# Kernel optimization log

Hardware: AMD Instinct MI355X
Metric: run time of the kernel (lower is better)

The kernel has to match this reference:

```python
import jax, jax.numpy as jnp
import numpy as np

N_NODES = 100000
N_EDGES = 1600000
N_FEAT = 100
HIDDEN = 64
N_CLASSES = 47


def setup_inputs() -> dict:
    key = jax.random.key(0)
    k1, k2, k3, k4 = jax.random.split(key, 4)
    x = jax.random.normal(k1, (N_NODES, N_FEAT), dtype=jnp.float32)
    edge_index = jax.random.randint(k2, (2, N_EDGES), 0, N_NODES, dtype=jnp.int64)
    # Glorot-style init for GCNConv weights; zero bias (PyG default)
    W0 = jax.random.normal(k3, (N_FEAT, HIDDEN), dtype=jnp.float32) * (1.0 / np.sqrt(N_FEAT))
    b0 = jnp.zeros((HIDDEN,), dtype=jnp.float32)
    W1 = jax.random.normal(k4, (HIDDEN, N_CLASSES), dtype=jnp.float32) * (1.0 / np.sqrt(HIDDEN))
    b1 = jnp.zeros((N_CLASSES,), dtype=jnp.float32)
    return {"x": x, "edge_index": edge_index, "W0": W0, "b0": b0, "W1": W1, "b1": b1}


def _gcn_norm(edge_index, n_nodes):
    # PyG gcn_norm with add_self_loops=True, edge_weight=1
    loop = jnp.arange(n_nodes, dtype=edge_index.dtype)
    row = jnp.concatenate([edge_index[0], loop])  # source nodes
    col = jnp.concatenate([edge_index[1], loop])  # destination nodes
    ones = jnp.ones(row.shape[0], dtype=jnp.float32)
    deg = jax.ops.segment_sum(ones, col, num_segments=n_nodes)
    dinv = jnp.where(deg > 0, jax.lax.rsqrt(deg), 0.0)
    norm = dinv[row] * dinv[col]  # [E + N]
    return row, col, norm


def _gcn_conv(x, W, b, row, col, norm, n_nodes):
    # GCNConv: transform, then gather-scale-scatter aggregate, then bias
    xw = x @ W                                   # [N, out]
    msg = norm[:, None] * xw[row]                # [E+N, out]
    out = jax.ops.segment_sum(msg, col, num_segments=n_nodes)
    return out + b


def reference(x, edge_index, W0, b0, W1, b1):
    n_nodes = x.shape[0]
    row, col, norm = _gcn_norm(edge_index, n_nodes)  # same graph -> same norm per layer (cached)
    h = _gcn_conv(x, W0, b0, row, col, norm, n_nodes)
    h = jax.nn.relu(h)  # dropout is identity in eval mode
    out = _gcn_conv(h, W1, b1, row, col, norm, n_nodes)
    return out
```

## Files before the change

### kernel.cpp

```cpp
#include <hip/hip_runtime.h>
#include <hip/hip_fp16.h>

#define N_NODES   100000
#define N_EDGES   1600000
#define N_FEAT    100
#define HIDDEN    64
#define N_CLASSES 47
#define ZPAD      48
#define NBIN      ((N_NODES + 255) / 256)
#define SBLK      512
#define CHUNK     (N_EDGES / SBLK)
#define NHIST     (NBIN * SBLK)
#define WT0_ELEMS (HIDDEN * 128)
#define WT1_ELEMS (ZPAD * 64)
#define WPREP_N   (WT0_ELEMS + WT1_ELEMS)

typedef _Float16 f16x8 __attribute__((ext_vector_type(8)));
typedef float f32x4 __attribute__((ext_vector_type(4)));


__global__ __launch_bounds__(512) void k_gscan1(const int* __restrict__ in,
                                                int* __restrict__ out,
                                                int* __restrict__ sums, int n) {
    __shared__ int tmp[512];
    int i = blockIdx.x * 512 + threadIdx.x;
    int v = (i < n) ? in[i] : 0;
    tmp[threadIdx.x] = v;
    __syncthreads();
    for (int off = 1; off < 512; off <<= 1) {
        int t = (threadIdx.x >= off) ? tmp[threadIdx.x - off] : 0;
        __syncthreads();
        tmp[threadIdx.x] += t;
        __syncthreads();
    }
    if (i < n) out[i] = tmp[threadIdx.x] - v;
    if (threadIdx.x == 511) sums[blockIdx.x] = tmp[511];
}

__global__ __launch_bounds__(512) void k_gscan2(int* __restrict__ sums, int nb) {
    __shared__ int tmp[512];
    int i = threadIdx.x;
    int v = (i < nb) ? sums[i] : 0;
    tmp[i] = v;
    __syncthreads();
    for (int off = 1; off < 512; off <<= 1) {
        int t = (i >= off) ? tmp[i - off] : 0;
        __syncthreads();
        tmp[i] += t;
        __syncthreads();
    }
    if (i < nb) sums[i] = tmp[i] - v;
}


__global__ __launch_bounds__(256) void k_hist(const int* __restrict__ ecol,
                                              int* __restrict__ gh,
                                              const float* __restrict__ W0,
                                              const float* __restrict__ W1,
                                              __half* __restrict__ wt0,
                                              __half* __restrict__ wt1) {
    int wi = blockIdx.x * 256 + threadIdx.x;
    if (wi < WT0_ELEMS) {
        int n = wi >> 7, k = wi & 127;
        wt0[wi] = __float2half((k < N_FEAT) ? W0[k * HIDDEN + n] : 0.0f);
    } else if (wi < WPREP_N) {
        int j = wi - WT0_ELEMS;
        int n = j >> 6, k = j & 63;
        wt1[j] = __float2half((n < N_CLASSES) ? W1[k * N_CLASSES + n] : 0.0f);
    }

    __shared__ int lh[NBIN];
    int b = blockIdx.x, t = threadIdx.x;
    for (int i = t; i < NBIN; i += 256) lh[i] = 0;
    __syncthreads();
    int e0 = b * CHUNK;
    for (int i = t; i < CHUNK; i += 256)
        atomicAdd(&lh[ecol[e0 + i] >> 8], 1);
    __syncthreads();
    for (int i = t; i < NBIN; i += 256) gh[i * SBLK + b] = lh[i];
}

__global__ __launch_bounds__(256) void k_radix_scatter(
    const int* __restrict__ erow, const int* __restrict__ ecol,
    const int* __restrict__ gpos, const int* __restrict__ hsums,
    int* __restrict__ pairs) {
    __shared__ int lc[NBIN];
    int b = blockIdx.x, t = threadIdx.x;
    for (int i = t; i < NBIN; i += 256) lc[i] = gpos[i * SBLK + b] + hsums[i];
    __syncthreads();
    int e0 = b * CHUNK;
    for (int i = t; i < CHUNK; i += 256) {
        int e = e0 + i;
        int r = erow[e], c = ecol[e];
        int pos = atomicAdd(&lc[c >> 8], 1);
        pairs[pos] = r | ((c & 255) << 17);
    }
}

__global__ __launch_bounds__(1024) void k_binfinish(
    const int* __restrict__ gpos, const int* __restrict__ hsums,
    const int* __restrict__ pairs,
    int* __restrict__ rp, float* __restrict__ dinv, int* __restrict__ eidx) {
    __shared__ int cnt[256];
    __shared__ int tmp[256];
    int b = blockIdx.x, t = threadIdx.x;
    int n0 = b << 8;
    int beg = gpos[b * SBLK] + hsums[b];
    int end = (b + 1 < NBIN) ? gpos[(b + 1) * SBLK] + hsums[b + 1] : N_EDGES;

    if (t < 256) cnt[t] = 0;
    __syncthreads();
    for (int i = beg + t; i < end; i += 1024)
        atomicAdd(&cnt[(pairs[i] >> 17) & 255], 1);
    __syncthreads();
    int v = 0;
    if (t < 256) { v = cnt[t]; tmp[t] = v; }
    __syncthreads();
    for (int off = 1; off < 256; off <<= 1) {
        int u = (t < 256 && t >= off) ? tmp[t - off] : 0;
        __syncthreads();
        if (t < 256) tmp[t] += u;
        __syncthreads();
    }
    if (t < 256) {
        int rpv = beg + tmp[t] - v;
        int n = n0 + t;
        if (n < N_NODES) {
            rp[n] = rpv;
            dinv[n] = rsqrtf(1.0f + (float)v);
        }
        cnt[t] = rpv;
    }
    if (b == NBIN - 1 && t == 0) rp[N_NODES] = N_EDGES;
    __syncthreads();
    for (int i = beg + t; i < end; i += 1024) {
        int p = pairs[i];
        int pos = atomicAdd(&cnt[(p >> 17) & 255], 1);
        eidx[pos] = p & 0x1FFFF;
    }
}

__global__ __launch_bounds__(256) void k_gemm1(
    const float* __restrict__ x, const __half* __restrict__ wt0,
    const float* __restrict__ dinv, __half* __restrict__ yh) {
    int w = threadIdx.x >> 6, l = threadIdx.x & 63;
    int g = l >> 4, c16 = l & 15;
    int row = blockIdx.x * 64 + w * 16 + c16;
    int rl = (row < N_NODES) ? row : (N_NODES - 1);
    const float* xr = x + (size_t)rl * N_FEAT;

    f16x8 a[4];
    #pragma unroll
    for (int s = 0; s < 4; ++s) {
        int k0 = 32 * s + 8 * g;
        float4 f0 = (k0 + 3 < N_FEAT) ? *(const float4*)(xr + k0)
                                      : make_float4(0.f, 0.f, 0.f, 0.f);
        float4 f1 = (k0 + 7 < N_FEAT) ? *(const float4*)(xr + k0 + 4)
                                      : make_float4(0.f, 0.f, 0.f, 0.f);
        a[s][0] = (_Float16)f0.x; a[s][1] = (_Float16)f0.y;
        a[s][2] = (_Float16)f0.z; a[s][3] = (_Float16)f0.w;
        a[s][4] = (_Float16)f1.x; a[s][5] = (_Float16)f1.y;
        a[s][6] = (_Float16)f1.z; a[s][7] = (_Float16)f1.w;
    }
    f32x4 acc0 = {0,0,0,0}, acc1 = {0,0,0,0}, acc2 = {0,0,0,0}, acc3 = {0,0,0,0};
    #pragma unroll
    for (int s = 0; s < 4; ++s) {
        int ko = 32 * s + 8 * g;
        f16x8 b0 = *(const f16x8*)(wt0 + (0 * 16 + c16) * 128 + ko);
        f16x8 b1 = *(const f16x8*)(wt0 + (1 * 16 + c16) * 128 + ko);
        f16x8 b2 = *(const f16x8*)(wt0 + (2 * 16 + c16) * 128 + ko);
        f16x8 b3 = *(const f16x8*)(wt0 + (3 * 16 + c16) * 128 + ko);
        acc0 = __builtin_amdgcn_mfma_f32_16x16x32_f16(a[s], b0, acc0, 0, 0, 0);
        acc1 = __builtin_amdgcn_mfma_f32_16x16x32_f16(a[s], b1, acc1, 0, 0, 0);
        acc2 = __builtin_amdgcn_mfma_f32_16x16x32_f16(a[s], b2, acc2, 0, 0, 0);
        acc3 = __builtin_amdgcn_mfma_f32_16x16x32_f16(a[s], b3, acc3, 0, 0, 0);
    }
    int orow = blockIdx.x * 64 + w * 16 + 4 * g;
    #pragma unroll
    for (int r = 0; r < 4; ++r) {
        int rr = orow + r;
        float di = (rr < N_NODES) ? dinv[rr] : 0.0f;
        size_t base = (size_t)rr * HIDDEN + c16;
        yh[base +  0] = __float2half(di * acc0[r]);
        yh[base + 16] = __float2half(di * acc1[r]);
        yh[base + 32] = __float2half(di * acc2[r]);
        yh[base + 48] = __float2half(di * acc3[r]);
    }
}

__global__ __launch_bounds__(256) void k_agg0(
    const int* __restrict__ rp, const int* __restrict__ eidx,
    const float* __restrict__ dinv, const __half* __restrict__ yh,
    const float* __restrict__ b0, const __half* __restrict__ wt1,
    __half* __restrict__ zh) {
    __shared__ __half hs[16][64];
    int t = blockIdx.x * 256 + threadIdx.x;
    int n = t >> 5;
    int hl = threadIdx.x & 31;
    int nl = threadIdx.x >> 5;

    ((__half2*)hs)[256 + threadIdx.x] = __floats2half2_rn(0.f, 0.f);

    int beg = rp[n], end = rp[n + 1];
    int deg = end - beg;
    int se = (beg + hl < end) ? eidx[beg + hl] : 0;
    const __half2* yh2 = (const __half2*)yh;
    float2 fs = __half22float2(yh2[(size_t)n * 32 + hl]);
    float ax = fs.x, ay = fs.y;
    int m = deg < 32 ? deg : 32;
    int base = threadIdx.x & 32;
    const __half2 hz = __floats2half2_rn(0.f, 0.f);

    {
        __half2 h[16];
        #pragma unroll
        for (int k = 0; k < 16; ++k) {
            int s = __shfl(se, base + k);
            h[k] = yh2[(size_t)s * 32 + hl];
        }
        #pragma unroll
        for (int k = 0; k < 16; ++k) h[k] = (m > k) ? h[k] : hz;
        #pragma unroll
        for (int s2 = 8; s2 >= 1; s2 >>= 1) {
            #pragma unroll
            for (int k = 0; k < s2; ++k) h[k] = __hadd2(h[2 * k], h[2 * k + 1]);
        }
        float2 bs = __half22float2(h[0]);
        ax += bs.x; ay += bs.y;
    }
    if (m > 16) {
        __half2 h[16];
        #pragma unroll
        for (int k = 0; k < 16; ++k) {
            int s = __shfl(se, base + 16 + k);
            h[k] = yh2[(size_t)s * 32 + hl];
        }
        #pragma unroll
        for (int k = 0; k < 16; ++k) h[k] = (m > 16 + k) ? h[k] : hz;
        #pragma unroll
        for (int s2 = 8; s2 >= 1; s2 >>= 1) {
            #pragma unroll
            for (int k = 0; k < s2; ++k) h[k] = __hadd2(h[2 * k], h[2 * k + 1]);
        }
        float2 bs = __half22float2(h[0]);
        ax += bs.x; ay += bs.y;
    }
    if (deg > 32) {
        for (int e = beg + 32; e < end; ++e) {
            int s = eidx[e];
            float2 fv = __half22float2(yh2[(size_t)s * 32 + hl]);
            ax += fv.x; ay += fv.y;
        }
    }
    float di = dinv[n];
    float2 b2 = ((const float2*)b0)[hl];
    float o0 = fmaxf(di * ax + b2.x, 0.0f);
    float o1 = fmaxf(di * ay + b2.y, 0.0f);
    ((__half2*)hs)[nl * 32 + hl] = __floats2half2_rn(o0, o1);
    __syncthreads();

    if (threadIdx.x < 64) {
        int l = threadIdx.x;
        int g = l >> 4, c16 = l & 15;
        f16x8 a0 = *(const f16x8*)(&hs[c16][8 * g]);
        f16x8 a1 = *(const f16x8*)(&hs[c16][32 + 8 * g]);
        f32x4 acc0 = {0,0,0,0}, acc1 = {0,0,0,0}, acc2 = {0,0,0,0};
        #pragma unroll
        for (int s = 0; s < 2; ++s) {
            int ko = 32 * s + 8 * g;
            f16x8 b0f = *(const f16x8*)(wt1 + (0 * 16 + c16) * 64 + ko);
            f16x8 b1f = *(const f16x8*)(wt1 + (1 * 16 + c16) * 64 + ko);
            f16x8 b2f = *(const f16x8*)(wt1 + (2 * 16 + c16) * 64 + ko);
            f16x8 av = s ? a1 : a0;
            acc0 = __builtin_amdgcn_mfma_f32_16x16x32_f16(av, b0f, acc0, 0, 0, 0);
            acc1 = __builtin_amdgcn_mfma_f32_16x16x32_f16(av, b1f, acc1, 0, 0, 0);
            acc2 = __builtin_amdgcn_mfma_f32_16x16x32_f16(av, b2f, acc2, 0, 0, 0);
        }
        if (g < 2) {
            int nrow = blockIdx.x * 8 + 4 * g;
            #pragma unroll
            for (int r = 0; r < 4; ++r) {
                float dr = dinv[nrow + r];
                size_t bz = (size_t)(nrow + r) * ZPAD + c16;
                zh[bz +  0] = __float2half(dr * acc0[r]);
                zh[bz + 16] = __float2half(dr * acc1[r]);
                zh[bz + 32] = __float2half(dr * acc2[r]);
            }
        }
    }
}

__global__ __launch_bounds__(256) void k_agg1(
    const int* __restrict__ rp, const int* __restrict__ eidx,
    const float* __restrict__ dinv, const __half* __restrict__ zh,
    const float* __restrict__ b1, float* __restrict__ out) {
    int t = blockIdx.x * 256 + threadIdx.x;
    int n = t >> 5;
    int hl = threadIdx.x & 31;
    if (n >= N_NODES) return;
    int beg = rp[n], end = rp[n + 1];
    int deg = end - beg;
    int se = (beg + hl < end) ? eidx[beg + hl] : 0;
    const __half2* zh2 = (const __half2*)zh;
    float ax = 0.0f, ay = 0.0f;
    if (hl < 24) {
        float2 f = __half22float2(zh2[(size_t)n * 24 + hl]);
        ax = f.x; ay = f.y;
    }
    int m = deg < 32 ? deg : 32;
    int base = threadIdx.x & 32;
    const __half2 hz = __floats2half2_rn(0.f, 0.f);

    {
        int sidx[16];
        #pragma unroll
        for (int k = 0; k < 16; ++k) sidx[k] = __shfl(se, base + k);
        if (hl < 24) {
            __half2 h[16];
            #pragma unroll
            for (int k = 0; k < 16; ++k) h[k] = zh2[(size_t)sidx[k] * 24 + hl];
            #pragma unroll
            for (int k = 0; k < 16; ++k) h[k] = (m > k) ? h[k] : hz;
            #pragma unroll
            for (int s2 = 8; s2 >= 1; s2 >>= 1) {
                #pragma unroll
                for (int k = 0; k < s2; ++k) h[k] = __hadd2(h[2 * k], h[2 * k + 1]);
            }
            float2 bs = __half22float2(h[0]);
            ax += bs.x; ay += bs.y;
        }
    }
    if (m > 16) {
        int sidx[16];
        #pragma unroll
        for (int k = 0; k < 16; ++k) sidx[k] = __shfl(se, base + 16 + k);
        if (hl < 24) {
            __half2 h[16];
            #pragma unroll
            for (int k = 0; k < 16; ++k) h[k] = zh2[(size_t)sidx[k] * 24 + hl];
            #pragma unroll
            for (int k = 0; k < 16; ++k) h[k] = (m > 16 + k) ? h[k] : hz;
            #pragma unroll
            for (int s2 = 8; s2 >= 1; s2 >>= 1) {
                #pragma unroll
                for (int k = 0; k < s2; ++k) h[k] = __hadd2(h[2 * k], h[2 * k + 1]);
            }
            float2 bs = __half22float2(h[0]);
            ax += bs.x; ay += bs.y;
        }
    }
    if (deg > 32) {
        for (int e = beg + 32; e < end; ++e) {
            int s = eidx[e];
            if (hl < 24) {
                float2 fv = __half22float2(zh2[(size_t)s * 24 + hl]);
                ax += fv.x; ay += fv.y;
            }
        }
    }
    if (hl < 24) {
        float di = dinv[n];
        out[(size_t)n * N_CLASSES + 2 * hl] = di * ax + b1[2 * hl];
        if (hl < 23)
            out[(size_t)n * N_CLASSES + 2 * hl + 1] = di * ay + b1[2 * hl + 1];
    }
}

extern "C" void kernel_launch(void* const* d_in, const int* in_sizes, int n_in,
                              void* d_out, int out_size, void* d_ws, size_t ws_size,
                              hipStream_t stream) {
    const float* x  = (const float*)d_in[0];
    const int*   ei = (const int*)d_in[1];
    const float* W0 = (const float*)d_in[2];
    const float* b0 = (const float*)d_in[3];
    const float* W1 = (const float*)d_in[4];
    const float* b1 = (const float*)d_in[5];
    float* out = (float*)d_out;

    char* ws = (char*)d_ws;
    float*  dinv  = (float*)(ws);
    int*    rp    = (int*)(ws + 412 * 1024);
    int*    hsums = (int*)(ws + 824 * 1024);
    int*    gh    = (int*)(ws + 828 * 1024);
    int*    gpos  = (int*)(ws + 1612 * 1024);
    __half* wt0   = (__half*)(ws + 2400 * 1024);
    __half* wt1   = (__half*)(ws + 2420 * 1024);
    int*    eidx  = (int*)(ws + 2428 * 1024);
    __half* yh    = (__half*)(ws + 10ull * 1024 * 1024);
    __half* zh    = (__half*)(ws + 23ull * 1024 * 1024);
    int*    pairs = (int*)zh;

    const int* erow = ei;
    const int* ecol = ei + N_EDGES;

    k_hist  <<<SBLK, 256, 0, stream>>>(ecol, gh, W0, W1, wt0, wt1);
    k_gscan1<<<NBIN, 512, 0, stream>>>(gh, gpos, hsums, NHIST);
    k_gscan2<<<1, 512, 0, stream>>>(hsums, NBIN);
    k_radix_scatter<<<SBLK, 256, 0, stream>>>(erow, ecol, gpos, hsums, pairs);
    k_binfinish<<<NBIN, 1024, 0, stream>>>(gpos, hsums, pairs, rp, dinv, eidx);

    k_gemm1<<<(N_NODES + 63) / 64, 256, 0, stream>>>(x, wt0, dinv, yh);
    k_agg0 <<<(N_NODES * 32) / 256, 256, 0, stream>>>(rp, eidx, dinv, yh, b0, wt1, zh);

    k_agg1 <<<(N_NODES * 32) / 256, 256, 0, stream>>>(rp, eidx, dinv, zh, b1, out);
}
```

Baseline: 131.4 us.

## Fold block-sum scan into consumers, pad z rows to 64 halves, widen scatter blocks

New measurement: 127.5 us (median of 2 runs). 3.0% less time.

```diff
diff --git a/kernel.cpp b/kernel.cpp
--- a/kernel.cpp
+++ b/kernel.cpp
@@ -6,13 +6,13 @@
 #define N_FEAT    100
 #define HIDDEN    64
 #define N_CLASSES 47
-#define ZPAD      48
+#define ZROWH     64
 #define NBIN      ((N_NODES + 255) / 256)
 #define SBLK      512
 #define CHUNK     (N_EDGES / SBLK)
 #define NHIST     (NBIN * SBLK)
 #define WT0_ELEMS (HIDDEN * 128)
-#define WT1_ELEMS (ZPAD * 64)
+#define WT1_ELEMS (48 * 64)
 #define WPREP_N   (WT0_ELEMS + WT1_ELEMS)
 
 typedef _Float16 f16x8 __attribute__((ext_vector_type(8)));
@@ -35,21 +35,6 @@
     }
     if (i < n) out[i] = tmp[threadIdx.x] - v;
     if (threadIdx.x == 511) sums[blockIdx.x] = tmp[511];
-}
-
-__global__ __launch_bounds__(512) void k_gscan2(int* __restrict__ sums, int nb) {
-    __shared__ int tmp[512];
-    int i = threadIdx.x;
-    int v = (i < nb) ? sums[i] : 0;
-    tmp[i] = v;
-    __syncthreads();
-    for (int off = 1; off < 512; off <<= 1) {
-        int t = (i >= off) ? tmp[i - off] : 0;
-        __syncthreads();
-        tmp[i] += t;
-        __syncthreads();
-    }
-    if (i < nb) sums[i] = tmp[i] - v;
 }
 
 
@@ -80,16 +65,26 @@
     for (int i = t; i < NBIN; i += 256) gh[i * SBLK + b] = lh[i];
 }
 
-__global__ __launch_bounds__(256) void k_radix_scatter(
+__global__ __launch_bounds__(512) void k_radix_scatter(
     const int* __restrict__ erow, const int* __restrict__ ecol,
-    const int* __restrict__ gpos, const int* __restrict__ hsums,
+    const int* __restrict__ gpos, const int* __restrict__ bsums,
     int* __restrict__ pairs) {
     __shared__ int lc[NBIN];
+    __shared__ int sc[512];
     int b = blockIdx.x, t = threadIdx.x;
-    for (int i = t; i < NBIN; i += 256) lc[i] = gpos[i * SBLK + b] + hsums[i];
+    int bv = (t < NBIN) ? bsums[t] : 0;
+    sc[t] = bv;
+    __syncthreads();
+    for (int off = 1; off < 512; off <<= 1) {
+        int u = (t >= off) ? sc[t - off] : 0;
+        __syncthreads();
+        sc[t] += u;
+        __syncthreads();
+    }
+    if (t < NBIN) lc[t] = gpos[t * SBLK + b] + sc[t] - bv;
     __syncthreads();
     int e0 = b * CHUNK;
-    for (int i = t; i < CHUNK; i += 256) {
+    for (int i = t; i < CHUNK; i += 512) {
         int e = e0 + i;
         int r = erow[e], c = ecol[e];
         int pos = atomicAdd(&lc[c >> 8], 1);
@@ -98,15 +93,27 @@
 }
 
 __global__ __launch_bounds__(1024) void k_binfinish(
-    const int* __restrict__ gpos, const int* __restrict__ hsums,
+    const int* __restrict__ gpos, const int* __restrict__ bsums,
     const int* __restrict__ pairs,
     int* __restrict__ rp, float* __restrict__ dinv, int* __restrict__ eidx) {
     __shared__ int cnt[256];
     __shared__ int tmp[256];
+    __shared__ int sc[512];
     int b = blockIdx.x, t = threadIdx.x;
     int n0 = b << 8;
-    int beg = gpos[b * SBLK] + hsums[b];
-    int end = (b + 1 < NBIN) ? gpos[(b + 1) * SBLK] + hsums[b + 1] : N_EDGES;
+    int bv = 0;
+    if (t < 512) { bv = (t < NBIN) ? bsums[t] : 0; sc[t] = bv; }
+    __syncthreads();
+    for (int off = 1; off < 512; off <<= 1) {
+        int u = (t < 512 && t >= off) ? sc[t - off] : 0;
+        __syncthreads();
+        if (t < 512) sc[t] += u;
+        __syncthreads();
+    }
+    if (t < 512) sc[t] -= bv;
+    __syncthreads();
+    int beg = gpos[b * SBLK] + sc[b];
+    int end = (b + 1 < NBIN) ? gpos[(b + 1) * SBLK] + sc[b + 1] : N_EDGES;
 
     if (t < 256) cnt[t] = 0;
     __syncthreads();
@@ -281,7 +288,7 @@
             #pragma unroll
             for (int r = 0; r < 4; ++r) {
                 float dr = dinv[nrow + r];
-                size_t bz = (size_t)(nrow + r) * ZPAD + c16;
+                size_t bz = (size_t)(nrow + r) * ZROWH + c16;
                 zh[bz +  0] = __float2half(dr * acc0[r]);
                 zh[bz + 16] = __float2half(dr * acc1[r]);
                 zh[bz + 32] = __float2half(dr * acc2[r]);
@@ -304,7 +311,7 @@
     const __half2* zh2 = (const __half2*)zh;
     float ax = 0.0f, ay = 0.0f;
     if (hl < 24) {
-        float2 f = __half22float2(zh2[(size_t)n * 24 + hl]);
+        float2 f = __half22float2(zh2[(size_t)n * 32 + hl]);
         ax = f.x; ay = f.y;
     }
     int m = deg < 32 ? deg : 32;
@@ -318,7 +325,7 @@
         if (hl < 24) {
             __half2 h[16];
             #pragma unroll
-            for (int k = 0; k < 16; ++k) h[k] = zh2[(size_t)sidx[k] * 24 + hl];
+            for (int k = 0; k < 16; ++k) h[k] = zh2[(size_t)sidx[k] * 32 + hl];
             #pragma unroll
             for (int k = 0; k < 16; ++k) h[k] = (m > k) ? h[k] : hz;
             #pragma unroll
@@ -337,7 +344,7 @@
         if (hl < 24) {
             __half2 h[16];
             #pragma unroll
-            for (int k = 0; k < 16; ++k) h[k] = zh2[(size_t)sidx[k] * 24 + hl];
+            for (int k = 0; k < 16; ++k) h[k] = zh2[(size_t)sidx[k] * 32 + hl];
             #pragma unroll
             for (int k = 0; k < 16; ++k) h[k] = (m > 16 + k) ? h[k] : hz;
             #pragma unroll
@@ -353,7 +360,7 @@
         for (int e = beg + 32; e < end; ++e) {
             int s = eidx[e];
             if (hl < 24) {
-                float2 fv = __half22float2(zh2[(size_t)s * 24 + hl]);
+                float2 fv = __half22float2(zh2[(size_t)s * 32 + hl]);
                 ax += fv.x; ay += fv.y;
             }
         }
@@ -380,7 +387,7 @@
     char* ws = (char*)d_ws;
     float*  dinv  = (float*)(ws);
     int*    rp    = (int*)(ws + 412 * 1024);
-    int*    hsums = (int*)(ws + 824 * 1024);
+    int*    bsums = (int*)(ws + 824 * 1024);
     int*    gh    = (int*)(ws + 828 * 1024);
     int*    gpos  = (int*)(ws + 1612 * 1024);
     __half* wt0   = (__half*)(ws + 2400 * 1024);
@@ -394,10 +401,9 @@
     const int* ecol = ei + N_EDGES;
 
     k_hist  <<<SBLK, 256, 0, stream>>>(ecol, gh, W0, W1, wt0, wt1);
-    k_gscan1<<<NBIN, 512, 0, stream>>>(gh, gpos, hsums, NHIST);
-    k_gscan2<<<1, 512, 0, stream>>>(hsums, NBIN);
-    k_radix_scatter<<<SBLK, 256, 0, stream>>>(erow, ecol, gpos, hsums, pairs);
-    k_binfinish<<<NBIN, 1024, 0, stream>>>(gpos, hsums, pairs, rp, dinv, eidx);
+    k_gscan1<<<NBIN, 512, 0, stream>>>(gh, gpos, bsums, NHIST);
+    k_radix_scatter<<<SBLK, 512, 0, stream>>>(erow, ecol, gpos, bsums, pairs);
+    k_binfinish<<<NBIN, 1024, 0, stream>>>(gpos, bsums, pairs, rp, dinv, eidx);
 
     k_gemm1<<<(N_NODES + 63) / 64, 256, 0, stream>>>(x, wt0, dinv, yh);
     k_agg0 <<<(N_NODES * 32) / 256, 256, 0, stream>>>(rp, eidx, dinv, yh, b0, wt1, zh);
```
